# Performance work log

Measured on AMD Instinct MI355X. Metric: run time of the kernel, lower is better.

## Reference

```python
import jax, jax.numpy as jnp
import numpy as np

EPS = 1e-5  # BatchNorm1d default eps


def setup_inputs() -> dict:
    key = jax.random.key(0)
    ks = jax.random.split(key, 8)
    B, N, C = 4, 4096, 512
    Ci = C // 2
    s = 1.0 / np.sqrt(C)
    si = 1.0 / np.sqrt(Ci)
    return {
        "x": jax.random.normal(ks[0], (B, N, C), jnp.float32),
        "gamma": jnp.ones((C,), jnp.float32),
        "beta": jnp.zeros((C,), jnp.float32),
        "theta_w": jax.random.normal(ks[1], (Ci, C), jnp.float32) * s,
        "theta_b": jnp.zeros((Ci,), jnp.float32),
        "phi_w": jax.random.normal(ks[2], (Ci, C), jnp.float32) * s,
        "phi_b": jnp.zeros((Ci,), jnp.float32),
        "g_w": jax.random.normal(ks[3], (Ci, C), jnp.float32) * s,
        "g_b": jnp.zeros((Ci,), jnp.float32),
        "w_w": jax.random.normal(ks[4], (C, Ci), jnp.float32) * si,
        "w_b": jnp.zeros((C,), jnp.float32),
    }


def reference(x, gamma, beta, theta_w, theta_b, phi_w, phi_b, g_w, g_b, w_w, w_b):
    # x: (B, N, C). BatchNorm1d in training mode: stats over batch and length dims.
    mean = jnp.mean(x, axis=(0, 1))                     # (C,)
    var = jnp.mean((x - mean) ** 2, axis=(0, 1))        # biased variance, (C,)
    feat = jax.nn.relu(gamma * (x - mean) * jax.lax.rsqrt(var + EPS) + beta)

    t = jnp.einsum('bnc,dc->bnd', feat, theta_w) + theta_b   # (B, N, Ci)
    p = jnp.einsum('bnc,dc->bnd', feat, phi_w) + phi_b       # (B, N, Ci)
    gx = jnp.einsum('bnc,dc->bnd', feat, g_w) + g_b          # (B, N, Ci)

    attn = jnp.einsum('bqd,bkd->bqk', t, p)             # unscaled QK^T, (B, N, N)
    attn = jax.nn.softmax(attn, axis=-1)
    y = jnp.einsum('bqk,bkd->bqd', attn, gx)            # (B, N, Ci)

    w_y = jnp.einsum('bnd,cd->bnc', y, w_w) + w_b       # (B, N, C)
    return x + w_y
```

## Files before the change

kernel.cpp:

```cpp
#include <hip/hip_runtime.h>

typedef unsigned short u16;
typedef __attribute__((ext_vector_type(4))) float f32x4;
typedef __attribute__((ext_vector_type(8))) _Float16 f16x8;
typedef __attribute__((ext_vector_type(8))) unsigned short u16x8;
typedef __attribute__((ext_vector_type(4))) unsigned short u16x4;

#define DEV __device__ __forceinline__

DEV u16 f2h(float f) {
    _Float16 h = (_Float16)f;
    u16 r;
    __builtin_memcpy(&r, &h, 2);
    return r;
}
DEV float h2f(u16 u) {
    _Float16 h;
    __builtin_memcpy(&h, &u, 2);
    return (float)h;
}

DEV f32x4 mfma16(f16x8 a, f16x8 b, f32x4 c) {
    return __builtin_amdgcn_mfma_f32_16x16x32_f16(a, b, c, 0, 0, 0);
}

DEV void gload16(const void* g, void* l) {
    __builtin_amdgcn_global_load_lds(
        (const __attribute__((address_space(1))) void*)g,
        (__attribute__((address_space(3))) void*)l, 16, 0, 0);
}

#define BB 4
#define NN 4096
#define CC 512
#define CI 256
#define RR (BB * NN)

#define OFF_FEAT 0u
#define OFF_Q    16777216u
#define OFF_K    25165824u
#define OFF_V    33554432u
#define OFF_Y    41943040u
#define OFF_WQKV 50331648u
#define OFF_WO   51118080u
#define OFF_BQKV 51380224u
#define OFF_PART 51383296u
#define OFF_SS   51907584u

__global__ void bn_partial(const float* __restrict__ x, float* __restrict__ part) {
    const int c = threadIdx.x;
    const int blk = blockIdx.x;
    const float* xp = x + (size_t)blk * 128 * CC + c;
    float s = 0.f, q = 0.f;
    for (int r = 0; r < 128; r++) {
        float v = xp[(size_t)r * CC];
        s += v; q += v * v;
    }
    part[blk * 1024 + c] = s;
    part[blk * 1024 + 512 + c] = q;
}

__global__ void prep_kernel(const float* __restrict__ part,
                            const float* __restrict__ gamma, const float* __restrict__ beta,
                            float* __restrict__ ss,
                            const float* __restrict__ thw, const float* __restrict__ phw,
                            const float* __restrict__ gw,
                            const float* __restrict__ thb, const float* __restrict__ phb,
                            const float* __restrict__ gb,
                            const float* __restrict__ ww,
                            u16* __restrict__ wqkv, u16* __restrict__ wo,
                            float* __restrict__ bqkv) {
    if (blockIdx.x == 1024) {
        const int c = threadIdx.x;
        float s = 0.f, q = 0.f;
        for (int i = 0; i < 128; i++) {
            s += part[i * 1024 + c];
            q += part[i * 1024 + 512 + c];
        }
        float m = s * (1.0f / (float)RR);
        float var = q * (1.0f / (float)RR) - m * m;
        float istd = rsqrtf(var + 1e-5f);
        float g = gamma[c] * istd;
        ss[c] = g;
        ss[512 + c] = beta[c] - m * g;
        return;
    }
    const int idx = blockIdx.x * 512 + threadIdx.x;
    if (idx < 768 * 512) {
        int row = idx >> 9, col = idx & 511;
        float v = (row < 256) ? thw[row * 512 + col]
                : (row < 512) ? phw[(row - 256) * 512 + col]
                              : gw[(row - 512) * 512 + col];
        wqkv[idx] = f2h(v);
    } else {
        int j = idx - 768 * 512;
        wo[j] = f2h(ww[j]);
    }
    if (idx < 768) {
        bqkv[idx] = (idx < 256) ? thb[idx] : (idx < 512) ? phb[idx - 256] : gb[idx - 512];
    }
}

template <int MODE>
__global__ __launch_bounds__(256) void gemm_bt(
    const u16* __restrict__ A, const float* __restrict__ X, const float* __restrict__ ss,
    const u16* __restrict__ Bm, int K,
    const float* __restrict__ bias, const float* __restrict__ xres,
    u16* __restrict__ oq, u16* __restrict__ okk, u16* __restrict__ ov,
    float* __restrict__ of) {
    __shared__ u16 As[128 * 32];
    __shared__ u16 Bs[128 * 32];
    const int tid = threadIdx.x;
    const int lane = tid & 63;
    const int l15 = lane & 15, kg = lane >> 4;
    const int wv = tid >> 6;
    const int wm = wv >> 1, wn = wv & 1;
    const int m0 = blockIdx.x * 128, n0 = blockIdx.y * 128;

    f32x4 acc[4][4];
    #pragma unroll
    for (int i = 0; i < 4; i++)
        #pragma unroll
        for (int j = 0; j < 4; j++) acc[i][j] = (f32x4){0.f, 0.f, 0.f, 0.f};

    const int rowA = tid >> 2, colA = (tid & 3) * 8;
    for (int k0 = 0; k0 < K; k0 += 32) {
        if constexpr (MODE == 0) {
            const float* xa = X + (size_t)(m0 + rowA) * CC + k0 + colA;
            f32x4 xv0 = *(const f32x4*)(xa);
            f32x4 xv1 = *(const f32x4*)(xa + 4);
            f32x4 xv2 = *(const f32x4*)(xa + (size_t)64 * CC);
            f32x4 xv3 = *(const f32x4*)(xa + (size_t)64 * CC + 4);
            f32x4 sc0 = *(const f32x4*)(ss + k0 + colA);
            f32x4 sc1 = *(const f32x4*)(ss + k0 + colA + 4);
            f32x4 sh0 = *(const f32x4*)(ss + 512 + k0 + colA);
            f32x4 sh1 = *(const f32x4*)(ss + 512 + k0 + colA + 4);
            u16x8 a0, a1;
            #pragma unroll
            for (int e = 0; e < 4; e++) {
                a0[e]     = f2h(fmaxf(xv0[e] * sc0[e] + sh0[e], 0.f));
                a0[4 + e] = f2h(fmaxf(xv1[e] * sc1[e] + sh1[e], 0.f));
                a1[e]     = f2h(fmaxf(xv2[e] * sc0[e] + sh0[e], 0.f));
                a1[4 + e] = f2h(fmaxf(xv3[e] * sc1[e] + sh1[e], 0.f));
            }
            *(u16x8*)&As[tid * 8] = a0;
            *(u16x8*)&As[2048 + tid * 8] = a1;
        } else {
            gload16(A + (size_t)(m0 + rowA) * K + k0 + colA, &As[tid * 8]);
            gload16(A + (size_t)(m0 + 64 + rowA) * K + k0 + colA, &As[2048 + tid * 8]);
        }
        gload16(Bm + (size_t)(n0 + rowA) * K + k0 + colA, &Bs[tid * 8]);
        gload16(Bm + (size_t)(n0 + 64 + rowA) * K + k0 + colA, &Bs[2048 + tid * 8]);
        __syncthreads();
        f16x8 af[4], bfr[4];
        #pragma unroll
        for (int i = 0; i < 4; i++)
            af[i] = *(const f16x8*)&As[(wm * 64 + i * 16 + l15) * 32 + kg * 8];
        #pragma unroll
        for (int i = 0; i < 4; i++)
            bfr[i] = *(const f16x8*)&Bs[(wn * 64 + i * 16 + l15) * 32 + kg * 8];
        #pragma unroll
        for (int mi = 0; mi < 4; mi++)
            #pragma unroll
            for (int ni = 0; ni < 4; ni++)
                acc[mi][ni] = mfma16(af[mi], bfr[ni], acc[mi][ni]);
        __syncthreads();
    }

    #pragma unroll
    for (int mi = 0; mi < 4; mi++) {
        #pragma unroll
        for (int ni = 0; ni < 4; ni++) {
            #pragma unroll
            for (int r = 0; r < 4; r++) {
                int row = m0 + wm * 64 + mi * 16 + kg * 4 + r;
                int col = n0 + wn * 64 + ni * 16 + l15;
                float v = acc[mi][ni][r];
                if constexpr (MODE == 0) {
                    v += bias[col];
                    u16 hv = f2h(v);
                    if (n0 < 256) {
                        oq[(size_t)row * CI + col] = hv;
                    } else if (n0 < 512) {
                        okk[(size_t)row * CI + (col - 256)] = hv;
                    } else {
                        int d = col - 512;
                        int bi = row >> 12, key = row & (NN - 1);
                        int k5 = key & 31;
                        int skey = (key & ~31) |
                                   ((((k5 >> 2) & 3) << 3) | (k5 & 3) | (((k5 >> 4) & 1) << 2));
                        ov[((size_t)bi * CI + d) * NN + skey] = hv;
                    }
                } else {
                    size_t o = (size_t)row * 512 + col;
                    of[o] = xres[o] + v + bias[col];
                }
            }
        }
    }
}

#define KVB 32
#define NSPLIT 4
#define KEYS_PER (NN / NSPLIT)
#define NTILE (KEYS_PER / KVB)
#define ATTN_LDS 65536

__global__ __launch_bounds__(256, 2) void attn_kernel(
    const u16* __restrict__ Qg, const u16* __restrict__ Kg,
    const u16* __restrict__ Vtg, u16* __restrict__ po01, u16* __restrict__ po23,
    float* __restrict__ ml) {
    extern __shared__ u16 smem[];

    const int tid = threadIdx.x, lane = tid & 63, wv = tid >> 6;
    const int l15 = lane & 15, kg = lane >> 4;
    const int sid = (blockIdx.x & 7) * 64 + (blockIdx.x >> 3);
    const int qt = sid & 31;
    const int b = (sid >> 5) & 3;
    const int sp = sid >> 7;
    const int kvoff = sp * KEYS_PER;
    const size_t kvbase = (size_t)b * NN * CI;
    const size_t vbase = (size_t)b * CI * NN;

    f16x8 qf[2][8];
    {
        const u16* qp0 = Qg + ((size_t)b * NN + qt * 128 + wv * 32 + l15) * CI + kg * 8;
        #pragma unroll
        for (int qs = 0; qs < 2; qs++)
            #pragma unroll
            for (int kk = 0; kk < 8; kk++)
                qf[qs][kk] = *(const f16x8*)(qp0 + (size_t)qs * 16 * CI + kk * 32);
    }

    f32x4 acc[16][2];
    #pragma unroll
    for (int i = 0; i < 16; i++)
        #pragma unroll
        for (int qs = 0; qs < 2; qs++) acc[i][qs] = (f32x4){0.f, 0.f, 0.f, 0.f};
    float mrow[2] = {-1e30f, -1e30f}, lrow[2] = {0.f, 0.f};

    const int chunk = tid & 31, rb = tid >> 5;
    const u16* ksrc[4];
    int kdst[4];
    #pragma unroll
    for (int i = 0; i < 4; i++) {
        int row = i * 8 + rb;
        int sc = chunk ^ (row & 7);
        ksrc[i] = Kg + kvbase + (size_t)(kvoff + KVB + row) * CI + sc * 8;
        kdst[i] = row * 256 + chunk * 8;
    }
    const int vc = tid & 3, vdb = tid >> 2;
    const u16* vsrc[4];
    int vdst[4];
    #pragma unroll
    for (int i = 0; i < 4; i++) {
        int d = i * 64 + vdb;
        int sc = vc ^ ((d >> 1) & 3);
        vsrc[i] = Vtg + vbase + (size_t)d * NN + kvoff + KVB + sc * 8;
        vdst[i] = d * KVB + vc * 8;
    }

    #pragma unroll
    for (int i = 0; i < 4; i++) {
        int row = i * 8 + rb;
        int sc = chunk ^ (row & 7);
        gload16(Kg + kvbase + (size_t)(kvoff + row) * CI + sc * 8, smem + kdst[i]);
    }
    #pragma unroll
    for (int i = 0; i < 4; i++) {
        int d = i * 64 + vdb;
        int sc = vc ^ ((d >> 1) & 3);
        gload16(Vtg + vbase + (size_t)d * NN + kvoff + sc * 8, smem + 16384 + vdst[i]);
    }
    __syncthreads();

    for (int it = 0; it < NTILE; ++it) {
        const int cur = (it & 1) * 8192;
        const u16* Ks = smem + cur;
        const u16* Vt = smem + 16384 + cur;
        if (it + 1 < NTILE) {
            const int nxt = cur ^ 8192;
            #pragma unroll
            for (int i = 0; i < 4; i++) {
                gload16(ksrc[i], smem + nxt + kdst[i]);
                ksrc[i] += KVB * CI;
            }
            #pragma unroll
            for (int i = 0; i < 4; i++) {
                gload16(vsrc[i], smem + 16384 + nxt + vdst[i]);
                vsrc[i] += KVB;
            }
        }

        f32x4 s[2][2];
        #pragma unroll
        for (int qs = 0; qs < 2; qs++)
            #pragma unroll
            for (int nt = 0; nt < 2; nt++) s[qs][nt] = (f32x4){0.f, 0.f, 0.f, 0.f};
        __builtin_amdgcn_s_setprio(1);
        #pragma unroll
        for (int kk = 0; kk < 8; kk++) {
            #pragma unroll
            for (int nt = 0; nt < 2; nt++) {
                int krow = nt * 16 + l15;
                f16x8 kf = *(const f16x8*)&Ks[krow * 256 + (((kk * 4 + kg) ^ (krow & 7)) << 3)];
                s[0][nt] = mfma16(kf, qf[0][kk], s[0][nt]);
                s[1][nt] = mfma16(kf, qf[1][kk], s[1][nt]);
            }
        }
        __builtin_amdgcn_s_setprio(0);

        float mx[2];
        #pragma unroll
        for (int qs = 0; qs < 2; qs++) {
            float m8 = fmaxf(fmaxf(fmaxf(s[qs][0][0], s[qs][0][1]), fmaxf(s[qs][0][2], s[qs][0][3])),
                             fmaxf(fmaxf(s[qs][1][0], s[qs][1][1]), fmaxf(s[qs][1][2], s[qs][1][3])));
            m8 = fmaxf(m8, __shfl_xor(m8, 16));
            m8 = fmaxf(m8, __shfl_xor(m8, 32));
            mx[qs] = m8;
        }
        float need = fmaxf(mx[0] - mrow[0], mx[1] - mrow[1]);
        if (!__all(need <= 8.f)) {
            float sclv[2];
            #pragma unroll
            for (int qs = 0; qs < 2; qs++) {
                float mnew = fmaxf(mrow[qs], mx[qs]);
                sclv[qs] = __expf(mrow[qs] - mnew);
                lrow[qs] *= sclv[qs];
                mrow[qs] = mnew;
            }
            #pragma unroll
            for (int qs = 0; qs < 2; qs++)
                #pragma unroll
                for (int r = 0; r < 4; r++) {
                    float sr = __shfl(sclv[qs], (lane & 48) | (kg * 4 + r), 64);
                    #pragma unroll
                    for (int dt = 0; dt < 16; dt++) acc[dt][qs][r] *= sr;
                }
        }
        f16x8 pa[2];
        #pragma unroll
        for (int qs = 0; qs < 2; qs++) {
            float rs = 0.f;
            #pragma unroll
            for (int nt = 0; nt < 2; nt++)
                #pragma unroll
                for (int r = 0; r < 4; r++) {
                    float p = __expf(s[qs][nt][r] - mrow[qs]);
                    rs += p;
                    pa[qs][nt * 4 + r] = (_Float16)p;
                }
            rs += __shfl_xor(rs, 16);
            rs += __shfl_xor(rs, 32);
            lrow[qs] += rs;
        }

        __builtin_amdgcn_s_setprio(1);
        #pragma unroll
        for (int dt = 0; dt < 16; dt++) {
            int d = dt * 16 + l15;
            f16x8 vf = *(const f16x8*)&Vt[d * KVB + ((kg ^ ((l15 >> 1) & 3)) << 3)];
            acc[dt][0] = mfma16(pa[0], vf, acc[dt][0]);
            acc[dt][1] = mfma16(pa[1], vf, acc[dt][1]);
        }
        __builtin_amdgcn_s_setprio(0);

        __syncthreads();
    }

    const int row0 = b * NN + qt * 128 + wv * 32;
    u16* pod = (sp < 2) ? (po01 + (size_t)sp * RR * CI)
                        : (po23 + (size_t)(sp - 2) * RR * CI);
    #pragma unroll
    for (int qs = 0; qs < 2; qs++)
        #pragma unroll
        for (int r = 0; r < 4; r++) {
            float li = __shfl(lrow[qs], (lane & 48) | (kg * 4 + r), 64);
            float inv = 1.f / li;
            int row = row0 + qs * 16 + kg * 4 + r;
            #pragma unroll
            for (int dt = 0; dt < 16; dt++)
                pod[(size_t)row * CI + dt * 16 + l15] = f2h(acc[dt][qs][r] * inv);
        }
    if (kg == 0) {
        #pragma unroll
        for (int qs = 0; qs < 2; qs++) {
            int row = row0 + qs * 16 + l15;
            ml[row * 8 + sp * 2] = mrow[qs];
            ml[row * 8 + sp * 2 + 1] = lrow[qs];
        }
    }
}

__global__ void attn_combine(const u16* __restrict__ po01, const u16* __restrict__ po23,
                             const float* __restrict__ ml, u16* __restrict__ yb) {
    const int gid = blockIdx.x * 256 + threadIdx.x;
    const int row = gid >> 6;
    const int d0 = (gid & 63) * 4;
    f32x4 ml0 = ((const f32x4*)ml)[row * 2];
    f32x4 ml1 = ((const f32x4*)ml)[row * 2 + 1];
    float m = fmaxf(fmaxf(ml0[0], ml0[2]), fmaxf(ml1[0], ml1[2]));
    float c0 = __expf(ml0[0] - m) * ml0[1];
    float c1 = __expf(ml0[2] - m) * ml0[3];
    float c2 = __expf(ml1[0] - m) * ml1[1];
    float c3 = __expf(ml1[2] - m) * ml1[3];
    float inv = 1.f / (c0 + c1 + c2 + c3);
    const size_t off = (size_t)row * CI + d0;
    const size_t spstride = (size_t)RR * CI;
    u16x4 p0 = *(const u16x4*)(po01 + off);
    u16x4 p1 = *(const u16x4*)(po01 + spstride + off);
    u16x4 p2 = *(const u16x4*)(po23 + off);
    u16x4 p3 = *(const u16x4*)(po23 + spstride + off);
    u16x4 o;
    #pragma unroll
    for (int e = 0; e < 4; e++)
        o[e] = f2h((c0 * h2f(p0[e]) + c1 * h2f(p1[e]) +
                    c2 * h2f(p2[e]) + c3 * h2f(p3[e])) * inv);
    *(u16x4*)(yb + off) = o;
}

extern "C" void kernel_launch(void* const* d_in, const int* in_sizes, int n_in,
                              void* d_out, int out_size, void* d_ws, size_t ws_size,
                              hipStream_t stream) {
    (void)in_sizes; (void)n_in; (void)out_size; (void)ws_size;
    const float* x     = (const float*)d_in[0];
    const float* gamma = (const float*)d_in[1];
    const float* beta  = (const float*)d_in[2];
    const float* thw   = (const float*)d_in[3];
    const float* thb   = (const float*)d_in[4];
    const float* phw   = (const float*)d_in[5];
    const float* phb   = (const float*)d_in[6];
    const float* gw    = (const float*)d_in[7];
    const float* gb    = (const float*)d_in[8];
    const float* ww    = (const float*)d_in[9];
    const float* wb    = (const float*)d_in[10];

    char* ws = (char*)d_ws;
    u16* po01  = (u16*)(ws + OFF_FEAT);
    u16* qb    = (u16*)(ws + OFF_Q);
    u16* kb    = (u16*)(ws + OFF_K);
    u16* vtb   = (u16*)(ws + OFF_V);
    u16* yb    = (u16*)(ws + OFF_Y);
    u16* wqkv  = (u16*)(ws + OFF_WQKV);
    u16* wo    = (u16*)(ws + OFF_WO);
    float* bqkv = (float*)(ws + OFF_BQKV);
    float* part = (float*)(ws + OFF_PART);
    float* ss   = (float*)(ws + OFF_SS);
    float* out  = (float*)d_out;
    u16* po23  = (u16*)d_out;

    (void)hipFuncSetAttribute((const void*)attn_kernel,
                              hipFuncAttributeMaxDynamicSharedMemorySize, ATTN_LDS);

    bn_partial<<<128, 512, 0, stream>>>(x, part);
    prep_kernel<<<1025, 512, 0, stream>>>(part, gamma, beta, ss,
                                          thw, phw, gw, thb, phb, gb, ww, wqkv, wo, bqkv);
    gemm_bt<0><<<dim3(128, 6), 256, 0, stream>>>(nullptr, x, ss, wqkv, 512, bqkv, nullptr,
                                                 qb, kb, vtb, nullptr);
    attn_kernel<<<512, 256, ATTN_LDS, stream>>>(qb, kb, vtb, po01, po23, part);
    attn_combine<<<RR * CI / 4 / 256, 256, 0, stream>>>(po01, po23, part, yb);
    gemm_bt<1><<<dim3(128, 4), 256, 0, stream>>>(yb, nullptr, nullptr, wo, 256, wb, x,
                                                 nullptr, nullptr, nullptr, out);
}
```

Measured before the change: 162.0 us.

## Widen GEMM N-tile to 256, split BN stats finer, vectorize combine

The projection GEMMs now use 128x256 output tiles, so each wave computes 4x8 MFMA tiles and the X-side normalization and A-tile loads are amortized over twice as many columns, halving grid.y. BN partial sums use 256 blocks of 64 rows instead of 128 of 128 for more parallelism, with the partials moved to the Y buffer region, which is still unused at that point. The attention combine kernel processes 8 elements per thread with 16-byte loads. Risks are higher register pressure from 32 accumulators, which could lower occupancy, and fewer GEMM blocks (384 and 256) to fill the CUs.

```diff
diff --git a/kernel.cpp b/kernel.cpp
--- a/kernel.cpp
+++ b/kernel.cpp
@@ -50,9 +50,9 @@
 __global__ void bn_partial(const float* __restrict__ x, float* __restrict__ part) {
     const int c = threadIdx.x;
     const int blk = blockIdx.x;
-    const float* xp = x + (size_t)blk * 128 * CC + c;
+    const float* xp = x + (size_t)blk * 64 * CC + c;
     float s = 0.f, q = 0.f;
-    for (int r = 0; r < 128; r++) {
+    for (int r = 0; r < 64; r++) {
         float v = xp[(size_t)r * CC];
         s += v; q += v * v;
     }
@@ -73,7 +73,7 @@
     if (blockIdx.x == 1024) {
         const int c = threadIdx.x;
         float s = 0.f, q = 0.f;
-        for (int i = 0; i < 128; i++) {
+        for (int i = 0; i < 256; i++) {
             s += part[i * 1024 + c];
             q += part[i * 1024 + 512 + c];
         }
@@ -109,19 +109,19 @@
     u16* __restrict__ oq, u16* __restrict__ okk, u16* __restrict__ ov,
     float* __restrict__ of) {
     __shared__ u16 As[128 * 32];
-    __shared__ u16 Bs[128 * 32];
+    __shared__ u16 Bs[256 * 32];
     const int tid = threadIdx.x;
     const int lane = tid & 63;
     const int l15 = lane & 15, kg = lane >> 4;
     const int wv = tid >> 6;
     const int wm = wv >> 1, wn = wv & 1;
-    const int m0 = blockIdx.x * 128, n0 = blockIdx.y * 128;
-
-    f32x4 acc[4][4];
+    const int m0 = blockIdx.x * 128, n0 = blockIdx.y * 256;
+
+    f32x4 acc[4][8];
     #pragma unroll
     for (int i = 0; i < 4; i++)
         #pragma unroll
-        for (int j = 0; j < 4; j++) acc[i][j] = (f32x4){0.f, 0.f, 0.f, 0.f};
+        for (int j = 0; j < 8; j++) acc[i][j] = (f32x4){0.f, 0.f, 0.f, 0.f};
 
     const int rowA = tid >> 2, colA = (tid & 3) * 8;
     for (int k0 = 0; k0 < K; k0 += 32) {
@@ -149,39 +149,40 @@
             gload16(A + (size_t)(m0 + rowA) * K + k0 + colA, &As[tid * 8]);
             gload16(A + (size_t)(m0 + 64 + rowA) * K + k0 + colA, &As[2048 + tid * 8]);
         }
-        gload16(Bm + (size_t)(n0 + rowA) * K + k0 + colA, &Bs[tid * 8]);
-        gload16(Bm + (size_t)(n0 + 64 + rowA) * K + k0 + colA, &Bs[2048 + tid * 8]);
+        #pragma unroll
+        for (int j = 0; j < 4; j++)
+            gload16(Bm + (size_t)(n0 + j * 64 + rowA) * K + k0 + colA,
+                    &Bs[j * 2048 + tid * 8]);
         __syncthreads();
-        f16x8 af[4], bfr[4];
+        f16x8 af[4];
         #pragma unroll
         for (int i = 0; i < 4; i++)
             af[i] = *(const f16x8*)&As[(wm * 64 + i * 16 + l15) * 32 + kg * 8];
         #pragma unroll
-        for (int i = 0; i < 4; i++)
-            bfr[i] = *(const f16x8*)&Bs[(wn * 64 + i * 16 + l15) * 32 + kg * 8];
-        #pragma unroll
-        for (int mi = 0; mi < 4; mi++)
-            #pragma unroll
-            for (int ni = 0; ni < 4; ni++)
-                acc[mi][ni] = mfma16(af[mi], bfr[ni], acc[mi][ni]);
+        for (int ni = 0; ni < 8; ni++) {
+            f16x8 bfr = *(const f16x8*)&Bs[(wn * 128 + ni * 16 + l15) * 32 + kg * 8];
+            #pragma unroll
+            for (int mi = 0; mi < 4; mi++)
+                acc[mi][ni] = mfma16(af[mi], bfr, acc[mi][ni]);
+        }
         __syncthreads();
     }
 
     #pragma unroll
     for (int mi = 0; mi < 4; mi++) {
         #pragma unroll
-        for (int ni = 0; ni < 4; ni++) {
+        for (int ni = 0; ni < 8; ni++) {
             #pragma unroll
             for (int r = 0; r < 4; r++) {
                 int row = m0 + wm * 64 + mi * 16 + kg * 4 + r;
-                int col = n0 + wn * 64 + ni * 16 + l15;
+                int col = n0 + wn * 128 + ni * 16 + l15;
                 float v = acc[mi][ni][r];
                 if constexpr (MODE == 0) {
                     v += bias[col];
                     u16 hv = f2h(v);
-                    if (n0 < 256) {
+                    if (col < 256) {
                         oq[(size_t)row * CI + col] = hv;
-                    } else if (n0 < 512) {
+                    } else if (col < 512) {
                         okk[(size_t)row * CI + (col - 256)] = hv;
                     } else {
                         int d = col - 512;
@@ -395,8 +396,8 @@
 __global__ void attn_combine(const u16* __restrict__ po01, const u16* __restrict__ po23,
                              const float* __restrict__ ml, u16* __restrict__ yb) {
     const int gid = blockIdx.x * 256 + threadIdx.x;
-    const int row = gid >> 6;
-    const int d0 = (gid & 63) * 4;
+    const int row = gid >> 5;
+    const int d0 = (gid & 31) * 8;
     f32x4 ml0 = ((const f32x4*)ml)[row * 2];
     f32x4 ml1 = ((const f32x4*)ml)[row * 2 + 1];
     float m = fmaxf(fmaxf(ml0[0], ml0[2]), fmaxf(ml1[0], ml1[2]));
@@ -407,16 +408,16 @@
     float inv = 1.f / (c0 + c1 + c2 + c3);
     const size_t off = (size_t)row * CI + d0;
     const size_t spstride = (size_t)RR * CI;
-    u16x4 p0 = *(const u16x4*)(po01 + off);
-    u16x4 p1 = *(const u16x4*)(po01 + spstride + off);
-    u16x4 p2 = *(const u16x4*)(po23 + off);
-    u16x4 p3 = *(const u16x4*)(po23 + spstride + off);
-    u16x4 o;
-    #pragma unroll
-    for (int e = 0; e < 4; e++)
+    u16x8 p0 = *(const u16x8*)(po01 + off);
+    u16x8 p1 = *(const u16x8*)(po01 + spstride + off);
+    u16x8 p2 = *(const u16x8*)(po23 + off);
+    u16x8 p3 = *(const u16x8*)(po23 + spstride + off);
+    u16x8 o;
+    #pragma unroll
+    for (int e = 0; e < 8; e++)
         o[e] = f2h((c0 * h2f(p0[e]) + c1 * h2f(p1[e]) +
                     c2 * h2f(p2[e]) + c3 * h2f(p3[e])) * inv);
-    *(u16x4*)(yb + off) = o;
+    *(u16x8*)(yb + off) = o;
 }
 
 extern "C" void kernel_launch(void* const* d_in, const int* in_sizes, int n_in,
@@ -444,7 +445,8 @@
     u16* wqkv  = (u16*)(ws + OFF_WQKV);
     u16* wo    = (u16*)(ws + OFF_WO);
     float* bqkv = (float*)(ws + OFF_BQKV);
-    float* part = (float*)(ws + OFF_PART);
+    float* bnpart = (float*)(ws + OFF_Y);
+    float* mlp  = (float*)(ws + OFF_PART);
     float* ss   = (float*)(ws + OFF_SS);
     float* out  = (float*)d_out;
     u16* po23  = (u16*)d_out;
@@ -452,13 +454,13 @@
     (void)hipFuncSetAttribute((const void*)attn_kernel,
                               hipFuncAttributeMaxDynamicSharedMemorySize, ATTN_LDS);
 
-    bn_partial<<<128, 512, 0, stream>>>(x, part);
-    prep_kernel<<<1025, 512, 0, stream>>>(part, gamma, beta, ss,
+    bn_partial<<<256, 512, 0, stream>>>(x, bnpart);
+    prep_kernel<<<1025, 512, 0, stream>>>(bnpart, gamma, beta, ss,
                                           thw, phw, gw, thb, phb, gb, ww, wqkv, wo, bqkv);
-    gemm_bt<0><<<dim3(128, 6), 256, 0, stream>>>(nullptr, x, ss, wqkv, 512, bqkv, nullptr,
+    gemm_bt<0><<<dim3(128, 3), 256, 0, stream>>>(nullptr, x, ss, wqkv, 512, bqkv, nullptr,
                                                  qb, kb, vtb, nullptr);
-    attn_kernel<<<512, 256, ATTN_LDS, stream>>>(qb, kb, vtb, po01, po23, part);
-    attn_combine<<<RR * CI / 4 / 256, 256, 0, stream>>>(po01, po23, part, yb);
-    gemm_bt<1><<<dim3(128, 4), 256, 0, stream>>>(yb, nullptr, nullptr, wo, 256, wb, x,
+    attn_kernel<<<512, 256, ATTN_LDS, stream>>>(qb, kb, vtb, po01, po23, mlp);
+    attn_combine<<<RR * CI / 8 / 256, 256, 0, stream>>>(po01, po23, mlp, yb);
+    gemm_bt<1><<<dim3(128, 2), 256, 0, stream>>>(yb, nullptr, nullptr, wo, 256, wb, x,
                                                  nullptr, nullptr, nullptr, out);
 }
```

Measured after the change: 209.0 us. +29.0%, slower.
